# Performance work log

Hardware: AMD Instinct MI355X
Metric: run time of the kernel (lower is better)

Reference implementation:

```python
import jax, jax.numpy as jnp
import numpy as np

N_NODES = 100000
EMB = 128
E = 800000


def _gcn_conv(x, W, b, src, dst, n_nodes):
    # PyG GCNConv: add self-loops, symmetric normalization D^-1/2 A D^-1/2,
    # linear transform, scatter-add aggregation onto target nodes, + bias.
    ones = jnp.ones(src.shape[0], dtype=x.dtype)
    deg = jax.ops.segment_sum(ones, dst, num_segments=n_nodes) + 1.0  # +1 for self-loop
    dinv = jnp.where(deg > 0, jax.lax.rsqrt(deg), 0.0)
    norm = dinv[src] * dinv[dst]                       # [E]
    h = x @ W                                          # [N, D]
    msg = norm[:, None] * h[src]                       # gather + scale, [E, D]
    out = jax.ops.segment_sum(msg, dst, num_segments=n_nodes)
    out = out + (dinv * dinv)[:, None] * h             # self-loop contribution
    return out + b


def setup_inputs() -> dict:
    key = jax.random.key(0)
    k = jax.random.split(key, 8)
    x = jax.random.normal(k[0], (N_NODES, EMB), dtype=jnp.float32)
    pos_edge_index = jax.random.randint(k[1], (2, E), 0, N_NODES, dtype=jnp.int64)
    neg_edge_index = jax.random.randint(k[2], (2, E), 0, N_NODES, dtype=jnp.int64)
    s = 1.0 / np.sqrt(EMB)
    W0 = jax.random.uniform(k[3], (EMB, EMB), jnp.float32, -s, s)
    b0 = jnp.zeros((EMB,), jnp.float32)
    W1 = jax.random.uniform(k[4], (EMB, EMB), jnp.float32, -s, s)
    b1 = jnp.zeros((EMB,), jnp.float32)
    return {"x": x, "W0": W0, "b0": b0, "W1": W1, "b1": b1,
            "pos_edge_index": pos_edge_index, "neg_edge_index": neg_edge_index}


def reference(x, W0, b0, W1, b1, pos_edge_index, neg_edge_index):
    edge_index = jnp.concatenate([pos_edge_index, neg_edge_index], axis=1)
    src, dst = edge_index[0], edge_index[1]
    z = _gcn_conv(x, W0, b0, src, dst, N_NODES)
    z = _gcn_conv(z, W1, b1, src, dst, N_NODES)
    return z
```

## Files before the change

kernel.cpp:

```cpp
#include <hip/hip_runtime.h>

#define N_NODES 100000
#define EMB 128
#define NE 800000
#define NEDGES (2 * NE)

#define NWIN 256
#define WNODES 391
#define WCAP 8192
#define ACHUNK 8192
#define ABLOCKS ((NEDGES + ACHUNK - 1) / ACHUNK)
#define SEGCAP 7000

typedef __attribute__((ext_vector_type(8))) short bf16x8;
typedef __attribute__((ext_vector_type(4))) float f32x4;
typedef __attribute__((ext_vector_type(2))) float f32x2;


__device__ __forceinline__ unsigned short f2bf(float f) {
    unsigned u = __builtin_bit_cast(unsigned, f);
    u += 0x7FFFu + ((u >> 16) & 1u);
    return (unsigned short)(u >> 16);
}

__device__ __forceinline__ unsigned pk2bf(float lo, float hi) {
    return (unsigned)f2bf(lo) | ((unsigned)f2bf(hi) << 16);
}

__device__ __forceinline__ float bflo(unsigned u) { return __builtin_bit_cast(float, u << 16); }
__device__ __forceinline__ float bfhi(unsigned u) { return __builtin_bit_cast(float, u & 0xFFFF0000u); }

__device__ __forceinline__ f32x2 unpk2(unsigned u) {
    f32x2 r;
    r.x = bflo(u);
    r.y = bfhi(u);
    return r;
}

__global__ void binit_kernel(int* __restrict__ bcur) {
    int w = threadIdx.x;
    if (w < NWIN) bcur[w] = w * WCAP;
}


__global__ __launch_bounds__(256) void binA_kernel(const int* __restrict__ pos,
                                                   const int* __restrict__ neg,
                                                   int* __restrict__ bucket_cursor,
                                                   unsigned* __restrict__ ptmp) {
    __shared__ int lcnt[NWIN];
    __shared__ int lofs[NWIN];
    __shared__ int lcur[NWIN];
    __shared__ int gbase[NWIN];
    __shared__ int stmp[NWIN];
    __shared__ unsigned pbuf[ACHUNK];
    __shared__ unsigned char wbuf[ACHUNK];

    const int tid  = threadIdx.x;
    const int e0   = blockIdx.x * ACHUNK;
    const int ecnt = (NEDGES - e0 < ACHUNK) ? (NEDGES - e0) : ACHUNK;

    if (tid < NWIN) lcnt[tid] = 0;
    __syncthreads();

    for (int k = tid; k < ecnt; k += 256) {
        int i = e0 + k;
        int d = (i < NE) ? pos[NE + i] : neg[i];
        atomicAdd(&lcnt[d / WNODES], 1);
    }
    __syncthreads();

    if (tid < NWIN) stmp[tid] = lcnt[tid];
    __syncthreads();
    for (int off = 1; off < NWIN; off <<= 1) {
        int v = (tid < NWIN && tid >= off) ? stmp[tid - off] : 0;
        __syncthreads();
        if (tid < NWIN) stmp[tid] += v;
        __syncthreads();
    }
    if (tid < NWIN) {
        lofs[tid]  = stmp[tid] - lcnt[tid];
        lcur[tid]  = stmp[tid] - lcnt[tid];
        gbase[tid] = atomicAdd(&bucket_cursor[tid], lcnt[tid]);
    }
    __syncthreads();

    for (int k = tid; k < ecnt; k += 256) {
        int i = e0 + k;
        int s, d;
        if (i < NE) { s = pos[i];      d = pos[NE + i]; }
        else        { s = neg[i - NE]; d = neg[i]; }
        int w = d / WNODES;
        unsigned v = ((unsigned)(d - w * WNODES) << 17) | (unsigned)s;
        int lp = atomicAdd(&lcur[w], 1);
        pbuf[lp] = v;
        wbuf[lp] = (unsigned char)w;
    }
    __syncthreads();

    for (int k = tid; k < ecnt; k += 256) {
        int w = wbuf[k];
        ptmp[gbase[w] + (k - lofs[w])] = pbuf[k];
    }
}


__global__ __launch_bounds__(NWIN) void wscan_kernel(const int* __restrict__ bcur,
                                                     int* __restrict__ wbase) {
    __shared__ int sc[NWIN];
    const int tid = threadIdx.x;
    int t = bcur[tid] - tid * WCAP;
    sc[tid] = t;
    __syncthreads();
    for (int off = 1; off < NWIN; off <<= 1) {
        int v = (tid >= off) ? sc[tid - off] : 0;
        __syncthreads();
        sc[tid] += v;
        __syncthreads();
    }
    wbase[tid] = sc[tid] - t;
}


__global__ __launch_bounds__(1024) void binC_kernel(const int* __restrict__ bcur,
                                                    const int* __restrict__ wbase,
                                                    const unsigned* __restrict__ ptmp,
                                                    int* __restrict__ rowptr,
                                                    float* __restrict__ dinv) {
    __shared__ int cnt[WNODES];
    __shared__ int sc[512];

    const int w   = blockIdx.x;
    const int lo  = w * WNODES;
    const int hi  = (lo + WNODES < N_NODES) ? lo + WNODES : N_NODES;
    const int nn  = hi - lo;
    const int tot = bcur[w] - w * WCAP;
    const int tid = threadIdx.x;
    const unsigned* __restrict__ rp = ptmp + (size_t)w * WCAP;

    for (int k = tid; k < nn; k += 1024) cnt[k] = 0;
    __syncthreads();

    for (int k = tid; k < tot; k += 1024) {
        atomicAdd(&cnt[rp[k] >> 17], 1);
    }
    __syncthreads();

    if (tid < 512) sc[tid] = (tid < nn) ? cnt[tid] : 0;
    __syncthreads();
    for (int off = 1; off < 512; off <<= 1) {
        int v = (tid < 512 && tid >= off) ? sc[tid - off] : 0;
        __syncthreads();
        if (tid < 512) sc[tid] += v;
        __syncthreads();
    }

    const int b = wbase[w];
    if (tid < nn) {
        rowptr[lo + tid] = b + sc[tid] - cnt[tid];
        dinv[lo + tid]   = rsqrtf((float)cnt[tid] + 1.0f);
    }
    if (w == 0 && tid == 0) rowptr[N_NODES] = NEDGES;
}


__global__ __launch_bounds__(1024) void binB_kernel(const int* __restrict__ bcur,
                                                    const int* __restrict__ rowptr,
                                                    const float* __restrict__ dinv,
                                                    const unsigned* __restrict__ ptmp,
                                                    unsigned* __restrict__ colidx) {
    __shared__ unsigned colseg[SEGCAP];
    __shared__ int lcur[WNODES];
    __shared__ float dinvw[WNODES];

    const int w    = blockIdx.x;
    const int lo   = w * WNODES;
    const int hi   = (lo + WNODES < N_NODES) ? lo + WNODES : N_NODES;
    const int nn   = hi - lo;
    const int base = rowptr[lo];
    const int tot  = bcur[w] - w * WCAP;
    const int tid  = threadIdx.x;
    const unsigned* __restrict__ rp = ptmp + (size_t)w * WCAP;

    for (int k = tid; k < nn; k += 1024) {
        lcur[k]  = rowptr[lo + k] - base;
        dinvw[k] = dinv[lo + k];
    }
    __syncthreads();

    for (int k = tid; k < tot; k += 1024) {
        unsigned v = rp[k];
        int dl = v >> 17;
        int s  = (int)(v & 0x1FFFFu);
        float nrm = dinv[s] * dinvw[dl];
        unsigned u = __builtin_bit_cast(unsigned, nrm);
        unsigned nb = (u + 0x7FFFu + ((u >> 16) & 1u)) >> 16;
        int lp = atomicAdd(&lcur[dl], 1);
        if (lp < SEGCAP) colseg[lp] = (nb << 17) | (unsigned)s;
    }
    __syncthreads();

    for (int k = tid; k < tot; k += 1024) colidx[base + k] = colseg[k];
}


#define GROWS 64

template<bool BF16IN>
__global__ __launch_bounds__(256) void gemm_kernel(const void* __restrict__ Xin,
                                                   const float* __restrict__ W,
                                                   unsigned short* __restrict__ Hb) {
    __shared__ unsigned short Wb[128 * 128];

    const int tid  = threadIdx.x;
    const int row0 = blockIdx.x * GROWS;

    for (int i = tid * 4; i < 128 * 128; i += 256 * 4) {
        float4 v = *(const float4*)&W[i];
        int k = i >> 7;
        int c = i & 127;
        int ks = k >> 5;
        int kg = (k >> 3) & 3;
        int j  = k & 7;
        float vv[4] = {v.x, v.y, v.z, v.w};
#pragma unroll
        for (int q = 0; q < 4; ++q) {
            int cc   = c + q;
            int ct   = cc >> 4;
            int lane = (cc & 15) + 16 * kg;
            Wb[((ct * 4 + ks) * 64 + lane) * 8 + j] = f2bf(vv[q]);
        }
    }
    __syncthreads();

    const int wave = tid >> 6;
    const int lane = tid & 63;
    const int r    = lane & 15;
    const int kg   = lane >> 4;

    int row = row0 + wave * 16 + r;
    int rowc = (row < N_NODES) ? row : N_NODES - 1;

    bf16x8 a[4];
    if (BF16IN) {
        const unsigned short* Xb = (const unsigned short*)Xin;
#pragma unroll
        for (int ks = 0; ks < 4; ++ks) {
            a[ks] = *(const bf16x8*)&Xb[(size_t)rowc * EMB + ks * 32 + kg * 8];
        }
    } else {
        const float* Xf = (const float*)Xin;
#pragma unroll
        for (int ks = 0; ks < 4; ++ks) {
            const float4* p = (const float4*)&Xf[(size_t)rowc * EMB + ks * 32 + kg * 8];
            float4 u = p[0];
            float4 v = p[1];
            bf16x8 av;
            av[0] = (short)f2bf(u.x); av[1] = (short)f2bf(u.y);
            av[2] = (short)f2bf(u.z); av[3] = (short)f2bf(u.w);
            av[4] = (short)f2bf(v.x); av[5] = (short)f2bf(v.y);
            av[6] = (short)f2bf(v.z); av[7] = (short)f2bf(v.w);
            a[ks] = av;
        }
    }

    f32x4 acc[8];
#pragma unroll
    for (int ct = 0; ct < 8; ++ct) acc[ct] = (f32x4){0.f, 0.f, 0.f, 0.f};

#pragma unroll
    for (int ct = 0; ct < 8; ++ct) {
#pragma unroll
        for (int ks = 0; ks < 4; ++ks) {
            bf16x8 b = *(bf16x8*)&Wb[((ct * 4 + ks) * 64 + lane) * 8];
            acc[ct] = __builtin_amdgcn_mfma_f32_16x16x32_bf16(a[ks], b, acc[ct], 0, 0, 0);
        }
    }

    const int orow0 = row0 + wave * 16 + (lane >> 4) * 4;
    const int oc    = lane & 15;
#pragma unroll
    for (int reg = 0; reg < 4; ++reg) {
        int orow = orow0 + reg;
        if (orow < N_NODES) {
#pragma unroll
            for (int ct = 0; ct < 8; ++ct) {
                Hb[(size_t)orow * EMB + ct * 16 + oc] = f2bf(acc[ct][reg]);
            }
        }
    }
}


#define AGG_WAVES 4

template<bool STORE_BF16>
__global__ __launch_bounds__(256) void aggregate_kernel(const int* __restrict__ rowptr,
                                                        const unsigned* __restrict__ rec,
                                                        const unsigned* __restrict__ Hb32,
                                                        const float* __restrict__ dinv,
                                                        const float* __restrict__ bias,
                                                        void* __restrict__ outv) {
    const int wave = threadIdx.x >> 6;
    const int lane = threadIdx.x & 63;
    const int node = blockIdx.x * AGG_WAVES + wave;
    if (node >= N_NODES) return;

    const int sub  = lane >> 4;
    const int dl   = lane & 15;
    const unsigned dlo = (unsigned)(dl << 4);

    const int start = rowptr[node];
    const int end   = rowptr[node + 1];

    f32x2 acc2[4];
#pragma unroll
    for (int j = 0; j < 4; ++j) acc2[j] = (f32x2){0.f, 0.f};

    const char* __restrict__ hbase = (const char*)Hb32;

    for (int b = start; b < end; b += 64) {
        int li = b + lane;
        unsigned rl = 0;
        if (li < end) rl = rec[li];
        int nb = end - b; if (nb > 64) nb = 64;
        for (int i = 0; i < nb; i += 16) {
            unsigned rA = __shfl(rl, i + sub,      64);
            unsigned rB = __shfl(rl, i + 4 + sub,  64);
            unsigned rC = __shfl(rl, i + 8 + sub,  64);
            unsigned rD = __shfl(rl, i + 12 + sub, 64);
            float nA = __builtin_bit_cast(float, (rA >> 17) << 16);
            float nB = __builtin_bit_cast(float, (rB >> 17) << 16);
            float nC = __builtin_bit_cast(float, (rC >> 17) << 16);
            float nD = __builtin_bit_cast(float, (rD >> 17) << 16);
            unsigned oA = ((rA & 0x1FFFFu) << 8) | dlo;
            unsigned oB = ((rB & 0x1FFFFu) << 8) | dlo;
            unsigned oC = ((rC & 0x1FFFFu) << 8) | dlo;
            unsigned oD = ((rD & 0x1FFFFu) << 8) | dlo;
            uint4 qA = *(const uint4*)(hbase + oA);
            uint4 qB = *(const uint4*)(hbase + oB);
            uint4 qC = *(const uint4*)(hbase + oC);
            uint4 qD = *(const uint4*)(hbase + oD);
            f32x2 nA2 = (f32x2){nA, nA};
            f32x2 nB2 = (f32x2){nB, nB};
            f32x2 nC2 = (f32x2){nC, nC};
            f32x2 nD2 = (f32x2){nD, nD};
            acc2[0] = __builtin_elementwise_fma(nA2, unpk2(qA.x), acc2[0]);
            acc2[1] = __builtin_elementwise_fma(nA2, unpk2(qA.y), acc2[1]);
            acc2[2] = __builtin_elementwise_fma(nA2, unpk2(qA.z), acc2[2]);
            acc2[3] = __builtin_elementwise_fma(nA2, unpk2(qA.w), acc2[3]);
            acc2[0] = __builtin_elementwise_fma(nB2, unpk2(qB.x), acc2[0]);
            acc2[1] = __builtin_elementwise_fma(nB2, unpk2(qB.y), acc2[1]);
            acc2[2] = __builtin_elementwise_fma(nB2, unpk2(qB.z), acc2[2]);
            acc2[3] = __builtin_elementwise_fma(nB2, unpk2(qB.w), acc2[3]);
            acc2[0] = __builtin_elementwise_fma(nC2, unpk2(qC.x), acc2[0]);
            acc2[1] = __builtin_elementwise_fma(nC2, unpk2(qC.y), acc2[1]);
            acc2[2] = __builtin_elementwise_fma(nC2, unpk2(qC.z), acc2[2]);
            acc2[3] = __builtin_elementwise_fma(nC2, unpk2(qC.w), acc2[3]);
            acc2[0] = __builtin_elementwise_fma(nD2, unpk2(qD.x), acc2[0]);
            acc2[1] = __builtin_elementwise_fma(nD2, unpk2(qD.y), acc2[1]);
            acc2[2] = __builtin_elementwise_fma(nD2, unpk2(qD.z), acc2[2]);
            acc2[3] = __builtin_elementwise_fma(nD2, unpk2(qD.w), acc2[3]);
        }
    }

    float acc[8];
#pragma unroll
    for (int j = 0; j < 4; ++j) { acc[2 * j] = acc2[j].x; acc[2 * j + 1] = acc2[j].y; }

#pragma unroll
    for (int j = 0; j < 8; ++j) {
        acc[j] += __shfl_xor(acc[j], 16, 64);
        acc[j] += __shfl_xor(acc[j], 32, 64);
    }

    if (sub == 0) {
        const float dd = dinv[node];
        const float s2 = dd * dd;
        uint4 q = *(const uint4*)(hbase + (((unsigned)node << 8) | dlo));
        acc[0] += s2 * bflo(q.x); acc[1] += s2 * bfhi(q.x);
        acc[2] += s2 * bflo(q.y); acc[3] += s2 * bfhi(q.y);
        acc[4] += s2 * bflo(q.z); acc[5] += s2 * bfhi(q.z);
        acc[6] += s2 * bflo(q.w); acc[7] += s2 * bfhi(q.w);

        float4 b0 = *(const float4*)&bias[dl * 8];
        float4 b1 = *(const float4*)&bias[dl * 8 + 4];
        float o[8];
        o[0] = acc[0] + b0.x; o[1] = acc[1] + b0.y; o[2] = acc[2] + b0.z; o[3] = acc[3] + b0.w;
        o[4] = acc[4] + b1.x; o[5] = acc[5] + b1.y; o[6] = acc[6] + b1.z; o[7] = acc[7] + b1.w;

        if (STORE_BF16) {
            unsigned short* ob = (unsigned short*)outv;
            uint4 pk;
            pk.x = pk2bf(o[0], o[1]);
            pk.y = pk2bf(o[2], o[3]);
            pk.z = pk2bf(o[4], o[5]);
            pk.w = pk2bf(o[6], o[7]);
            *(uint4*)&ob[(size_t)node * EMB + dl * 8] = pk;
        } else {
            float* of = (float*)outv;
            *(float4*)&of[(size_t)node * EMB + dl * 8]     = make_float4(o[0], o[1], o[2], o[3]);
            *(float4*)&of[(size_t)node * EMB + dl * 8 + 4] = make_float4(o[4], o[5], o[6], o[7]);
        }
    }
}


extern "C" void kernel_launch(void* const* d_in, const int* in_sizes, int n_in,
                              void* d_out, int out_size, void* d_ws, size_t ws_size,
                              hipStream_t stream) {
    const float* x  = (const float*)d_in[0];
    const float* W0 = (const float*)d_in[1];
    const float* b0 = (const float*)d_in[2];
    const float* W1 = (const float*)d_in[3];
    const float* b1 = (const float*)d_in[4];
    const int*   pos = (const int*)d_in[5];
    const int*   neg = (const int*)d_in[6];

    float* ws      = (float*)d_ws;
    float* dinv    = ws;
    unsigned short* hb = (unsigned short*)(ws + 100352);
    int*   rowptr  = (int*)(ws + 6500352);
    int*   bcur    = (int*)(ws + 6600356);
    int*   wbase   = (int*)(ws + 6600612);
    unsigned* ptmp = (unsigned*)(ws + 6600872);
    unsigned* colidx = (unsigned*)(ws + 8698024);
    unsigned short* zb = (unsigned short*)(ws + 10298024);

    binit_kernel<<<1, NWIN, 0, stream>>>(bcur);
    binA_kernel<<<ABLOCKS, 256, 0, stream>>>(pos, neg, bcur, ptmp);
    wscan_kernel<<<1, NWIN, 0, stream>>>(bcur, wbase);
    binC_kernel<<<NWIN, 1024, 0, stream>>>(bcur, wbase, ptmp, rowptr, dinv);
    binB_kernel<<<NWIN, 1024, 0, stream>>>(bcur, rowptr, dinv, ptmp, colidx);

    const int agg_grid  = (N_NODES + AGG_WAVES - 1) / AGG_WAVES;
    const int gemm_grid = (N_NODES + GROWS - 1) / GROWS;

    gemm_kernel<false><<<gemm_grid, 256, 0, stream>>>(x, W0, hb);
    aggregate_kernel<true><<<agg_grid, 256, 0, stream>>>(
        rowptr, colidx, (const unsigned*)hb, dinv, b0, zb);

    gemm_kernel<true><<<gemm_grid, 256, 0, stream>>>(zb, W1, hb);
    aggregate_kernel<false><<<agg_grid, 256, 0, stream>>>(
        rowptr, colidx, (const unsigned*)hb, dinv, b1, d_out);
}
```

Measured before the change: 240.0 us.

## Fuse CSR count and fill kernels; compute edge norm from dinv table in aggregation

Merges the binC and binB kernels into one, reusing the in-shared counts as write cursors so the ptmp window is read in a single launch. Column records no longer carry a bf16 norm. They store src+1, and the aggregation kernel gathers dinv[src] from a shifted table with a zero sentinel for padding, factoring dinv[dst] out to the epilogue. This removes a launch and the global dinv gather during CSR build, and improves norm precision. The cost is an extra scattered float load per edge in both aggregation passes and a branch for the sentinel.

```diff
diff --git a/kernel.cpp b/kernel.cpp
--- a/kernel.cpp
+++ b/kernel.cpp
@@ -121,13 +121,15 @@
 }
 
 
-__global__ __launch_bounds__(1024) void binC_kernel(const int* __restrict__ bcur,
-                                                    const int* __restrict__ wbase,
-                                                    const unsigned* __restrict__ ptmp,
-                                                    int* __restrict__ rowptr,
-                                                    float* __restrict__ dinv) {
+__global__ __launch_bounds__(1024) void binCB_kernel(const int* __restrict__ bcur,
+                                                     const int* __restrict__ wbase,
+                                                     const unsigned* __restrict__ ptmp,
+                                                     int* __restrict__ rowptr,
+                                                     float* __restrict__ dtab,
+                                                     unsigned* __restrict__ colidx) {
     __shared__ int cnt[WNODES];
     __shared__ int sc[512];
+    __shared__ unsigned colseg[SEGCAP];
 
     const int w   = blockIdx.x;
     const int lo  = w * WNODES;
@@ -154,48 +156,25 @@
         __syncthreads();
     }
 
-    const int b = wbase[w];
+    const int base = wbase[w];
+    int myexc = 0;
     if (tid < nn) {
-        rowptr[lo + tid] = b + sc[tid] - cnt[tid];
-        dinv[lo + tid]   = rsqrtf((float)cnt[tid] + 1.0f);
-    }
-    if (w == 0 && tid == 0) rowptr[N_NODES] = NEDGES;
-}
-
-
-__global__ __launch_bounds__(1024) void binB_kernel(const int* __restrict__ bcur,
-                                                    const int* __restrict__ rowptr,
-                                                    const float* __restrict__ dinv,
-                                                    const unsigned* __restrict__ ptmp,
-                                                    unsigned* __restrict__ colidx) {
-    __shared__ unsigned colseg[SEGCAP];
-    __shared__ int lcur[WNODES];
-    __shared__ float dinvw[WNODES];
-
-    const int w    = blockIdx.x;
-    const int lo   = w * WNODES;
-    const int hi   = (lo + WNODES < N_NODES) ? lo + WNODES : N_NODES;
-    const int nn   = hi - lo;
-    const int base = rowptr[lo];
-    const int tot  = bcur[w] - w * WCAP;
-    const int tid  = threadIdx.x;
-    const unsigned* __restrict__ rp = ptmp + (size_t)w * WCAP;
-
-    for (int k = tid; k < nn; k += 1024) {
-        lcur[k]  = rowptr[lo + k] - base;
-        dinvw[k] = dinv[lo + k];
-    }
+        myexc = sc[tid] - cnt[tid];
+        rowptr[lo + tid]  = base + myexc;
+        dtab[lo + tid + 1] = rsqrtf((float)cnt[tid] + 1.0f);
+    }
+    if (w == 0 && tid == 0) { rowptr[N_NODES] = NEDGES; dtab[0] = 0.0f; }
+    __syncthreads();
+
+    if (tid < nn) cnt[tid] = myexc;
     __syncthreads();
 
     for (int k = tid; k < tot; k += 1024) {
         unsigned v = rp[k];
         int dl = v >> 17;
-        int s  = (int)(v & 0x1FFFFu);
-        float nrm = dinv[s] * dinvw[dl];
-        unsigned u = __builtin_bit_cast(unsigned, nrm);
-        unsigned nb = (u + 0x7FFFu + ((u >> 16) & 1u)) >> 16;
-        int lp = atomicAdd(&lcur[dl], 1);
-        if (lp < SEGCAP) colseg[lp] = (nb << 17) | (unsigned)s;
+        unsigned s = (v & 0x1FFFFu) + 1u;
+        int lp = atomicAdd(&cnt[dl], 1);
+        if (lp < SEGCAP) colseg[lp] = s;
     }
     __syncthreads();
 
@@ -297,7 +276,7 @@
 __global__ __launch_bounds__(256) void aggregate_kernel(const int* __restrict__ rowptr,
                                                         const unsigned* __restrict__ rec,
                                                         const unsigned* __restrict__ Hb32,
-                                                        const float* __restrict__ dinv,
+                                                        const float* __restrict__ dtab,
                                                         const float* __restrict__ bias,
                                                         void* __restrict__ outv) {
     const int wave = threadIdx.x >> 6;
@@ -328,14 +307,14 @@
             unsigned rB = __shfl(rl, i + 4 + sub,  64);
             unsigned rC = __shfl(rl, i + 8 + sub,  64);
             unsigned rD = __shfl(rl, i + 12 + sub, 64);
-            float nA = __builtin_bit_cast(float, (rA >> 17) << 16);
-            float nB = __builtin_bit_cast(float, (rB >> 17) << 16);
-            float nC = __builtin_bit_cast(float, (rC >> 17) << 16);
-            float nD = __builtin_bit_cast(float, (rD >> 17) << 16);
-            unsigned oA = ((rA & 0x1FFFFu) << 8) | dlo;
-            unsigned oB = ((rB & 0x1FFFFu) << 8) | dlo;
-            unsigned oC = ((rC & 0x1FFFFu) << 8) | dlo;
-            unsigned oD = ((rD & 0x1FFFFu) << 8) | dlo;
+            float nA = dtab[rA];
+            float nB = dtab[rB];
+            float nC = dtab[rC];
+            float nD = dtab[rD];
+            unsigned oA = rA ? (((rA - 1u) << 8) | dlo) : dlo;
+            unsigned oB = rB ? (((rB - 1u) << 8) | dlo) : dlo;
+            unsigned oC = rC ? (((rC - 1u) << 8) | dlo) : dlo;
+            unsigned oD = rD ? (((rD - 1u) << 8) | dlo) : dlo;
             uint4 qA = *(const uint4*)(hbase + oA);
             uint4 qB = *(const uint4*)(hbase + oB);
             uint4 qC = *(const uint4*)(hbase + oC);
@@ -374,19 +353,23 @@
     }
 
     if (sub == 0) {
-        const float dd = dinv[node];
+        const float dd = dtab[node + 1];
         const float s2 = dd * dd;
         uint4 q = *(const uint4*)(hbase + (((unsigned)node << 8) | dlo));
-        acc[0] += s2 * bflo(q.x); acc[1] += s2 * bfhi(q.x);
-        acc[2] += s2 * bflo(q.y); acc[3] += s2 * bfhi(q.y);
-        acc[4] += s2 * bflo(q.z); acc[5] += s2 * bfhi(q.z);
-        acc[6] += s2 * bflo(q.w); acc[7] += s2 * bfhi(q.w);
+        float o[8];
+        o[0] = dd * acc[0] + s2 * bflo(q.x);
+        o[1] = dd * acc[1] + s2 * bfhi(q.x);
+        o[2] = dd * acc[2] + s2 * bflo(q.y);
+        o[3] = dd * acc[3] + s2 * bfhi(q.y);
+        o[4] = dd * acc[4] + s2 * bflo(q.z);
+        o[5] = dd * acc[5] + s2 * bfhi(q.z);
+        o[6] = dd * acc[6] + s2 * bflo(q.w);
+        o[7] = dd * acc[7] + s2 * bfhi(q.w);
 
         float4 b0 = *(const float4*)&bias[dl * 8];
         float4 b1 = *(const float4*)&bias[dl * 8 + 4];
-        float o[8];
-        o[0] = acc[0] + b0.x; o[1] = acc[1] + b0.y; o[2] = acc[2] + b0.z; o[3] = acc[3] + b0.w;
-        o[4] = acc[4] + b1.x; o[5] = acc[5] + b1.y; o[6] = acc[6] + b1.z; o[7] = acc[7] + b1.w;
+        o[0] += b0.x; o[1] += b0.y; o[2] += b0.z; o[3] += b0.w;
+        o[4] += b1.x; o[5] += b1.y; o[6] += b1.z; o[7] += b1.w;
 
         if (STORE_BF16) {
             unsigned short* ob = (unsigned short*)outv;
@@ -417,7 +400,7 @@
     const int*   neg = (const int*)d_in[6];
 
     float* ws      = (float*)d_ws;
-    float* dinv    = ws;
+    float* dtab    = ws;
     unsigned short* hb = (unsigned short*)(ws + 100352);
     int*   rowptr  = (int*)(ws + 6500352);
     int*   bcur    = (int*)(ws + 6600356);
@@ -429,17 +412,16 @@
     binit_kernel<<<1, NWIN, 0, stream>>>(bcur);
     binA_kernel<<<ABLOCKS, 256, 0, stream>>>(pos, neg, bcur, ptmp);
     wscan_kernel<<<1, NWIN, 0, stream>>>(bcur, wbase);
-    binC_kernel<<<NWIN, 1024, 0, stream>>>(bcur, wbase, ptmp, rowptr, dinv);
-    binB_kernel<<<NWIN, 1024, 0, stream>>>(bcur, rowptr, dinv, ptmp, colidx);
+    binCB_kernel<<<NWIN, 1024, 0, stream>>>(bcur, wbase, ptmp, rowptr, dtab, colidx);
 
     const int agg_grid  = (N_NODES + AGG_WAVES - 1) / AGG_WAVES;
     const int gemm_grid = (N_NODES + GROWS - 1) / GROWS;
 
     gemm_kernel<false><<<gemm_grid, 256, 0, stream>>>(x, W0, hb);
     aggregate_kernel<true><<<agg_grid, 256, 0, stream>>>(
-        rowptr, colidx, (const unsigned*)hb, dinv, b0, zb);
+        rowptr, colidx, (const unsigned*)hb, dtab, b0, zb);
 
     gemm_kernel<true><<<gemm_grid, 256, 0, stream>>>(zb, W1, hb);
     aggregate_kernel<false><<<agg_grid, 256, 0, stream>>>(
-        rowptr, colidx, (const unsigned*)hb, dinv, b1, d_out);
-}
+        rowptr, colidx, (const unsigned*)hb, dtab, b1, d_out);
+}
```

Measured after the change: 235.5 us. About the same (-1.9%).
